# Performance work log

Hardware: AMD Instinct MI355X
Metric: run time of the kernel (lower is better)

## Reference

```python
import jax, jax.numpy as jnp
import numpy as np

B, S = 8192, 4096
EPS = 1e-6
ALPHA, BETA = 0.1, 0.1


def setup_inputs() -> dict:
    key = jax.random.key(0)
    k1, k2, k3, k4 = jax.random.split(key, 4)
    yhat = jax.random.normal(k1, (B, S), dtype=jnp.float32)
    y_dense = jax.random.normal(k2, (B, S), dtype=jnp.float32)
    keep = jax.random.bernoulli(k3, 0.5, (B, S))
    y = jnp.where(keep, y_dense, 0.0)
    # neighbor matrix: entries remapped {1.0->alpha, 2.0->beta}, mostly zero
    r = jax.random.randint(k4, (S, S), 0, 10)
    W = jnp.where(r == 1, ALPHA, jnp.where(r == 2, BETA, 0.0)).astype(jnp.float32)
    return {"yhat": yhat, "y": y, "W": W}


def reference(yhat, y, W):
    mask = (y != 0).astype(yhat.dtype)            # [B, S] nonzero-target mask
    sq = jnp.square(y - yhat)                      # [B, S] squared error
    # per-column loop `df_spatial_loss[:, i] = squared_error @ W[i]` == sq @ W.T
    spatial = sq @ W.T                             # [B, S] spatial regularization
    total = (sq + spatial) * mask                  # gather-at-nonzero == masking
    # mean over the nonzero entries only, then sqrt (RMSE)
    loss = jnp.sqrt(total.sum() / mask.sum() + EPS)
    return loss
```

## Files before the change

kernel.cpp:

```cpp
#include <hip/hip_runtime.h>
#include <math.h>

typedef unsigned long long u64;
typedef unsigned int u32;
typedef unsigned char u8;
typedef __attribute__((ext_vector_type(2))) unsigned long long u64x2;
typedef __attribute__((ext_vector_type(4))) int i32x4;

#define NB 8192
#define NS 4096

static const size_t OFF_CNT = 0;
static const size_t OFF_P3  = 16384;
static const size_t OFF_MB  = 32768;
static const size_t OFF_WB  = OFF_MB + (size_t)64 * 8192 * 8;
static const size_t OFF_M8  = 32768;
static const size_t OFF_BT  = OFF_M8 + (size_t)NB * NS;
static const size_t WS_NEED = OFF_BT + (size_t)NS * NS;

__device__ __forceinline__ void gload_lds16(const void* g, void* l) {
    __builtin_amdgcn_global_load_lds(
        (const __attribute__((address_space(1))) unsigned int*)g,
        (__attribute__((address_space(3))) unsigned int*)l, 16, 0, 0);
}


__global__ __launch_bounds__(256) void k1b_mask8(
    const float* __restrict__ y, u32* __restrict__ m8, u64* __restrict__ pcnt)
{
    __shared__ unsigned rc[4];
    const int t = threadIdx.x;
    const float4* y4 = (const float4*)y;
    size_t base = (size_t)blockIdx.x * 4096 + t;
    unsigned lcnt = 0;
    #pragma unroll 4
    for (int k = 0; k < 16; ++k) {
        float4 v = y4[base + (size_t)k * 256];
        unsigned b0 = v.x != 0.0f, b1 = v.y != 0.0f, b2 = v.z != 0.0f, b3 = v.w != 0.0f;
        lcnt += b0 + b1 + b2 + b3;
        m8[base + (size_t)k * 256] = b0 | (b1 << 8) | (b2 << 16) | (b3 << 24);
    }
    for (int off = 32; off; off >>= 1) lcnt += __shfl_down(lcnt, off, 64);
    if ((t & 63) == 0) rc[t >> 6] = lcnt;
    __syncthreads();
    if (t == 0) pcnt[blockIdx.x] = (u64)rc[0] + rc[1] + rc[2] + rc[3];
}

__global__ __launch_bounds__(256) void k2b_bt(
    const float* __restrict__ W, u32* __restrict__ bt)
{
    __shared__ float tile[64][65];
    const int j0 = blockIdx.x * 64, i0 = blockIdx.y * 64;
    const int t = threadIdx.x;
    #pragma unroll
    for (int k = 0; k < 16; ++k) {
        int lin = t + (k << 8);
        int r = lin >> 6, c = lin & 63;
        tile[r][c] = W[(size_t)(i0 + r) * NS + (j0 + c)];
    }
    __syncthreads();
    const int jj = t >> 2, ck = t & 3;
    u32 wd[4];
    #pragma unroll
    for (int g = 0; g < 4; ++g) {
        u32 u = 0;
        #pragma unroll
        for (int bb = 0; bb < 4; ++bb)
            u |= (tile[ck * 16 + g * 4 + bb][jj] != 0.0f ? 1u : 0u) << (8 * bb);
        wd[g] = u;
    }
    uint4 out = make_uint4(wd[0], wd[1], wd[2], wd[3]);
    *(uint4*)&bt[(((size_t)(j0 + jj) << 12) + (size_t)(i0 + ck * 16)) >> 2] = out;
}

__global__ __launch_bounds__(256) void k3b_mfma(
    const float* __restrict__ y, const float* __restrict__ yhat,
    const u8* __restrict__ m8, const u8* __restrict__ bt,
    double* __restrict__ p3)
{
    __shared__ alignas(16) u8 lds[2][16384];
    const int b0 = blockIdx.x << 7;
    const int j0 = blockIdx.y << 7;
    const int t = threadIdx.x, l = t & 63, wv = t >> 6;
    const int wr = wv >> 1, wc = wv & 1;

    const int row4 = t >> 2, pos = t & 3;
    const int chunk = pos ^ ((row4 >> 1) & 3);
    const u8* srcA = m8 + ((size_t)(b0 + row4) << 12) + ((size_t)chunk << 4);
    const u8* srcB = bt + ((size_t)(j0 + row4) << 12) + ((size_t)chunk << 4);

    const int slot = ((l >> 4) ^ ((l >> 1) & 3)) & 3;
    const int frbase = ((wr << 6) + (l & 15)) * 64 + (slot << 4);
    const int fcbase = 8192 + ((wc << 6) + (l & 15)) * 64 + (slot << 4);

    i32x4 acc[4][4];
    #pragma unroll
    for (int i = 0; i < 4; ++i)
        #pragma unroll
        for (int j = 0; j < 4; ++j) acc[i][j] = (i32x4){0, 0, 0, 0};

    auto stage = [&](int s, int buf) {
        const u8* sA = srcA + (s << 6);
        const u8* sB = srcB + (s << 6);
        u8* dA = &lds[buf][(size_t)wv << 10];
        u8* dB = &lds[buf][8192 + ((size_t)wv << 10)];
        gload_lds16(sA, dA);
        gload_lds16(sA + ((size_t)64 << 12), dA + 4096);
        gload_lds16(sB, dB);
        gload_lds16(sB + ((size_t)64 << 12), dB + 4096);
    };

    stage(0, 0);
    __syncthreads();

    #pragma unroll 1
    for (int ks = 0; ks < 64; ++ks) {
        const int cb = ks & 1;
        if (ks < 63) stage(ks + 1, cb ^ 1);
        const u8* L = lds[cb];
        i32x4 a[4], b[4];
        #pragma unroll
        for (int f = 0; f < 4; ++f) {
            a[f] = *(const i32x4*)&L[frbase + f * 1024];
            b[f] = *(const i32x4*)&L[fcbase + f * 1024];
        }
        #pragma unroll
        for (int fr = 0; fr < 4; ++fr)
            #pragma unroll
            for (int fc = 0; fc < 4; ++fc)
                acc[fr][fc] = __builtin_amdgcn_mfma_i32_16x16x64_i8(
                    a[fr], b[fc], acc[fr][fc], 0, 0, 0);
        __syncthreads();
    }

    float part = 0.0f;
    const int col = j0 + (wc << 6) + (l & 15);
    #pragma unroll
    for (int fr = 0; fr < 4; ++fr)
        #pragma unroll
        for (int q = 0; q < 4; ++q) {
            size_t rbase = ((size_t)(b0 + (wr << 6) + (fr << 4) + ((l >> 4) << 2) + q) << 12) + col;
            #pragma unroll
            for (int fc = 0; fc < 4; ++fc) {
                float yv = y[rbase + (fc << 4)];
                float hv = yhat[rbase + (fc << 4)];
                float e = yv - hv;
                float wgt = 0.1f * (float)acc[fr][fc][q] + (yv != 0.0f ? 1.0f : 0.0f);
                part = fmaf(e * e, wgt, part);
            }
        }

    for (int off = 32; off; off >>= 1) part += __shfl_down(part, off, 64);
    float* red = (float*)lds;
    __syncthreads();
    if ((t & 63) == 0) red[t >> 6] = part;
    __syncthreads();
    if (t == 0)
        p3[(size_t)blockIdx.y * gridDim.x + blockIdx.x] =
            (double)red[0] + (double)red[1] + (double)red[2] + (double)red[3];
}


__global__ __launch_bounds__(256) void k1_pack_mask(
    const float* __restrict__ y, u64* __restrict__ mbT, u64* __restrict__ pcnt)
{
    __shared__ unsigned rc[4];
    const unsigned t = threadIdx.x;
    const unsigned lane = t & 63;
    const float4* y4 = (const float4*)y;
    u64 qi = (u64)blockIdx.x * 256 + t;
    const u64 stride = (u64)2048 * 256;
    unsigned lcnt = 0;
    #pragma unroll 4
    for (int it = 0; it < 16; ++it, qi += stride) {
        float4 v = y4[qi];
        u64 b0 = __ballot(v.x != 0.0f);
        u64 b1 = __ballot(v.y != 0.0f);
        u64 b2 = __ballot(v.z != 0.0f);
        u64 b3 = __ballot(v.w != 0.0f);
        lcnt += (v.x != 0.0f) + (v.y != 0.0f) + (v.z != 0.0f) + (v.w != 0.0f);
        if (lane < 4) {
            unsigned sh = lane << 4;
            u64 word = ((b0 >> sh) & 0xFFFFull)
                     | (((b1 >> sh) & 0xFFFFull) << 16)
                     | (((b2 >> sh) & 0xFFFFull) << 32)
                     | (((b3 >> sh) & 0xFFFFull) << 48);
            u64 gw = ((qi - lane) >> 4) + lane;
            mbT[((gw & 63) << 13) + (gw >> 6)] = word;
        }
    }
    for (int off = 32; off; off >>= 1) lcnt += __shfl_down(lcnt, off, 64);
    if ((t & 63) == 0) rc[t >> 6] = lcnt;
    __syncthreads();
    if (t == 0) pcnt[blockIdx.x] = (u64)rc[0] + rc[1] + rc[2] + rc[3];
}

__global__ __launch_bounds__(256) void k2_pack_w(
    const float* __restrict__ W, u64* __restrict__ wbT)
{
    __shared__ float tile[64][65];
    const int j0 = blockIdx.x * 64;
    const int w  = blockIdx.y;
    const int i0 = w * 64;
    const int t = threadIdx.x;
    #pragma unroll
    for (int k = 0; k < 16; ++k) {
        int lin = t + (k << 8);
        int r = lin >> 6, c = lin & 63;
        tile[r][c] = W[(size_t)(i0 + r) * NS + (j0 + c)];
    }
    __syncthreads();
    const int lane = t & 63;
    const int wvv = t >> 6;
    const int pr = ((lane & 15) << 2) + (lane >> 4);
    for (int jj = wvv; jj < 64; jj += 4) {
        u64 bal = __ballot(tile[pr][jj] != 0.0f);
        if (lane == 0) wbT[((size_t)w << 12) + (j0 + jj)] = bal;
    }
}

__global__ __launch_bounds__(256) void k3_main(
    const float* __restrict__ y, const float* __restrict__ yhat,
    const u64* __restrict__ mbT, const u64* __restrict__ wbT,
    double* __restrict__ p3)
{
    __shared__ alignas(16) u64 mT[16 * 128];
    __shared__ alignas(16) u64 wT[16 * 128];
    const int b0 = blockIdx.x << 7;
    const int j0 = blockIdx.y << 7;
    const int t  = threadIdx.x;
    const int r0 = (t >> 4) << 3;
    const int cj = t & 15;
    const unsigned sx = ((unsigned)cj >> 2) << 4;

    unsigned cnt[8][8];
    #pragma unroll
    for (int a = 0; a < 8; ++a)
        #pragma unroll
        for (int b = 0; b < 8; ++b) cnt[a][b] = 0;

    char* mB = (char*)mT;
    char* wB = (char*)wT;

    #pragma unroll 1
    for (int s = 0; s < 4; ++s) {
        u64x2 gm[4], gq[4];
        #pragma unroll
        for (int k = 0; k < 4; ++k) {
            int lin = t + (k << 8);
            int wl = (s << 4) + (lin >> 6), c2 = lin & 63;
            gm[k] = *(const u64x2*)&mbT[((size_t)wl << 13) + b0 + 2 * c2];
            gq[k] = *(const u64x2*)&wbT[((size_t)wl << 12) + j0 + 2 * c2];
        }
        __syncthreads();
        #pragma unroll
        for (int k = 0; k < 4; ++k) {
            int lin = t + (k << 8);
            int wl = lin >> 6, c2 = lin & 63;
            int p = c2 ^ ((c2 >> 4) & 3);
            *(u64x2*)(mB + (wl << 10) + (c2 << 4)) = gm[k];
            *(u64x2*)(wB + (wl << 10) + (p << 4)) = gq[k];
        }
        __syncthreads();

        unsigned mo = (unsigned)(r0 << 3);
        unsigned qs = (unsigned)(cj << 6) + sx;
        #pragma unroll 2
        for (int w = 0; w < 16; ++w) {
            unsigned ml[16], ql[16];
            #pragma unroll
            for (int k = 0; k < 4; ++k) {
                uint4 a = *(const uint4*)(mB + mo + (k << 4));
                ml[4 * k + 0] = a.x; ml[4 * k + 1] = a.y;
                ml[4 * k + 2] = a.z; ml[4 * k + 3] = a.w;
                uint4 b = *(const uint4*)(wB + (qs ^ (unsigned)(k << 4)));
                ql[4 * k + 0] = b.x; ql[4 * k + 1] = b.y;
                ql[4 * k + 2] = b.z; ql[4 * k + 3] = b.w;
            }
            #pragma unroll
            for (int aa = 0; aa < 8; ++aa)
                #pragma unroll
                for (int bb = 0; bb < 8; ++bb) {
                    unsigned x0 = ml[2 * aa] & ql[2 * bb];
                    unsigned x1 = ml[2 * aa + 1] & ql[2 * bb + 1];
                    asm("v_bcnt_u32_b32 %0, %1, %0" : "+v"(cnt[aa][bb]) : "v"(x0));
                    asm("v_bcnt_u32_b32 %0, %1, %0" : "+v"(cnt[aa][bb]) : "v"(x1));
                }
            mo += 1024; qs += 1024;
        }
    }

    float part = 0.0f;
    const int c0 = cj << 3;
    #pragma unroll
    for (int aa = 0; aa < 8; ++aa) {
        size_t off = ((size_t)(b0 + r0 + aa) << 12) + (size_t)(j0 + c0);
        float ys[8], hs[8];
        *(float4*)&ys[0] = *(const float4*)(y + off);
        *(float4*)&ys[4] = *(const float4*)(y + off + 4);
        *(float4*)&hs[0] = *(const float4*)(yhat + off);
        *(float4*)&hs[4] = *(const float4*)(yhat + off + 4);
        #pragma unroll
        for (int bb = 0; bb < 8; ++bb) {
            float e = ys[bb] - hs[bb];
            float wgt = 0.1f * (float)cnt[aa][bb] + (ys[bb] != 0.0f ? 1.0f : 0.0f);
            part = fmaf(e * e, wgt, part);
        }
    }

    for (int off = 32; off; off >>= 1) part += __shfl_down(part, off, 64);
    float* red = (float*)mT;
    __syncthreads();
    if ((t & 63) == 0) red[t >> 6] = part;
    __syncthreads();
    if (t == 0)
        p3[(size_t)blockIdx.y * gridDim.x + blockIdx.x] =
            (double)red[0] + (double)red[1] + (double)red[2] + (double)red[3];
}

__global__ __launch_bounds__(256) void k4_final(
    const u64* __restrict__ pcnt, const double* __restrict__ p3, float* __restrict__ out)
{
    __shared__ double rs[4];
    __shared__ u64 rcc[4];
    double s3 = 0.0;
    u64 c = 0;
    for (int i = threadIdx.x; i < 2048; i += 256) { s3 += p3[i]; c += pcnt[i]; }
    for (int off = 32; off; off >>= 1) {
        s3 += __shfl_down(s3, off, 64);
        c  += __shfl_down(c, off, 64);
    }
    int wv = threadIdx.x >> 6;
    if ((threadIdx.x & 63) == 0) { rs[wv] = s3; rcc[wv] = c; }
    __syncthreads();
    if (threadIdx.x == 0) {
        double S3 = rs[0] + rs[1] + rs[2] + rs[3];
        double C  = (double)(rcc[0] + rcc[1] + rcc[2] + rcc[3]);
        out[0] = (float)sqrt(S3 / C + 1e-6);
    }
}

extern "C" void kernel_launch(void* const* d_in, const int* in_sizes, int n_in,
                              void* d_out, int out_size, void* d_ws, size_t ws_size,
                              hipStream_t stream) {
    const float* yhat = (const float*)d_in[0];
    const float* y    = (const float*)d_in[1];
    const float* W    = (const float*)d_in[2];
    char* ws = (char*)d_ws;
    u64*    pcnt = (u64*)(ws + OFF_CNT);
    double* p3   = (double*)(ws + OFF_P3);

    if (ws_size >= WS_NEED) {
        u32* m8 = (u32*)(ws + OFF_M8);
        u32* bt = (u32*)(ws + OFF_BT);
        k1b_mask8<<<dim3(2048), dim3(256), 0, stream>>>(y, m8, pcnt);
        k2b_bt<<<dim3(64, 64), dim3(256), 0, stream>>>(W, bt);
        k3b_mfma<<<dim3(64, 32), dim3(256), 0, stream>>>(
            y, yhat, (const u8*)m8, (const u8*)bt, p3);
        k4_final<<<dim3(1), dim3(256), 0, stream>>>(pcnt, p3, (float*)d_out);
    } else {
        u64* mbT = (u64*)(ws + OFF_MB);
        u64* wbT = (u64*)(ws + OFF_WB);
        k1_pack_mask<<<dim3(2048), dim3(256), 0, stream>>>(y, mbT, pcnt);
        k2_pack_w<<<dim3(64, 64), dim3(256), 0, stream>>>(W, wbT);
        k3_main<<<dim3(64, 32), dim3(256), 0, stream>>>(y, yhat, mbT, wbT, p3);
        k4_final<<<dim3(1), dim3(256), 0, stream>>>(pcnt, p3, (float*)d_out);
    }
}
```

Before: 226.2 us.

## Split output tiles between int8 MFMA and bit-popcount paths in one hybrid kernel

```diff
diff --git a/kernel.cpp b/kernel.cpp
--- a/kernel.cpp
+++ b/kernel.cpp
@@ -12,16 +12,284 @@
 
 static const size_t OFF_CNT = 0;
 static const size_t OFF_P3  = 16384;
-static const size_t OFF_MB  = 32768;
-static const size_t OFF_WB  = OFF_MB + (size_t)64 * 8192 * 8;
 static const size_t OFF_M8  = 32768;
 static const size_t OFF_BT  = OFF_M8 + (size_t)NB * NS;
-static const size_t WS_NEED = OFF_BT + (size_t)NS * NS;
+static const size_t WS_MFMA = OFF_BT + (size_t)NS * NS;
+static const size_t OFF_MBT = WS_MFMA;
+static const size_t OFF_WBT = OFF_MBT + (size_t)64 * NB * 8;
+static const size_t WS_HYB  = OFF_WBT + (size_t)64 * NS * 8;
 
 __device__ __forceinline__ void gload_lds16(const void* g, void* l) {
     __builtin_amdgcn_global_load_lds(
         (const __attribute__((address_space(1))) unsigned int*)g,
         (__attribute__((address_space(3))) unsigned int*)l, 16, 0, 0);
+}
+
+
+__global__ __launch_bounds__(256) void k1h(
+    const float* __restrict__ y, u32* __restrict__ m8,
+    u64* __restrict__ mbT, u64* __restrict__ pcnt)
+{
+    __shared__ unsigned rc[4];
+    const unsigned t = threadIdx.x;
+    const unsigned lane = t & 63;
+    const float4* y4 = (const float4*)y;
+    u64 qi = (u64)blockIdx.x * 256 + t;
+    const u64 stride = (u64)2048 * 256;
+    unsigned lcnt = 0;
+    #pragma unroll 4
+    for (int it = 0; it < 16; ++it, qi += stride) {
+        float4 v = y4[qi];
+        unsigned c0 = v.x != 0.0f, c1 = v.y != 0.0f, c2 = v.z != 0.0f, c3 = v.w != 0.0f;
+        u64 b0 = __ballot(v.x != 0.0f);
+        u64 b1 = __ballot(v.y != 0.0f);
+        u64 b2 = __ballot(v.z != 0.0f);
+        u64 b3 = __ballot(v.w != 0.0f);
+        lcnt += c0 + c1 + c2 + c3;
+        m8[qi] = c0 | (c1 << 8) | (c2 << 16) | (c3 << 24);
+        if (lane < 4) {
+            unsigned sh = lane << 4;
+            u64 word = ((b0 >> sh) & 0xFFFFull)
+                     | (((b1 >> sh) & 0xFFFFull) << 16)
+                     | (((b2 >> sh) & 0xFFFFull) << 32)
+                     | (((b3 >> sh) & 0xFFFFull) << 48);
+            u64 gw = ((qi - lane) >> 4) + lane;
+            mbT[((gw & 63) << 13) + (gw >> 6)] = word;
+        }
+    }
+    for (int off = 32; off; off >>= 1) lcnt += __shfl_down(lcnt, off, 64);
+    if ((t & 63) == 0) rc[t >> 6] = lcnt;
+    __syncthreads();
+    if (t == 0) pcnt[blockIdx.x] = (u64)rc[0] + rc[1] + rc[2] + rc[3];
+}
+
+__global__ __launch_bounds__(256) void k2h(
+    const float* __restrict__ W, u32* __restrict__ bt, u64* __restrict__ wbT)
+{
+    __shared__ float tile[64][65];
+    const int j0 = blockIdx.x * 64, w = blockIdx.y, i0 = w * 64;
+    const int t = threadIdx.x;
+    #pragma unroll
+    for (int k = 0; k < 16; ++k) {
+        int lin = t + (k << 8);
+        int r = lin >> 6, c = lin & 63;
+        tile[r][c] = W[(size_t)(i0 + r) * NS + (j0 + c)];
+    }
+    __syncthreads();
+    {
+        const int jj = t >> 2, ck = t & 3;
+        u32 wd[4];
+        #pragma unroll
+        for (int g = 0; g < 4; ++g) {
+            u32 u = 0;
+            #pragma unroll
+            for (int bb = 0; bb < 4; ++bb)
+                u |= (tile[ck * 16 + g * 4 + bb][jj] != 0.0f ? 1u : 0u) << (8 * bb);
+            wd[g] = u;
+        }
+        uint4 out = make_uint4(wd[0], wd[1], wd[2], wd[3]);
+        *(uint4*)&bt[(((size_t)(j0 + jj) << 12) + (size_t)(i0 + ck * 16)) >> 2] = out;
+    }
+    {
+        const int lane = t & 63;
+        const int wvv = t >> 6;
+        const int pr = ((lane & 15) << 2) + (lane >> 4);
+        for (int jj = wvv; jj < 64; jj += 4) {
+            u64 bal = __ballot(tile[pr][jj] != 0.0f);
+            if (lane == 0) wbT[((size_t)w << 12) + (j0 + jj)] = bal;
+        }
+    }
+}
+
+__global__ __launch_bounds__(256) void k3h(
+    const float* __restrict__ y, const float* __restrict__ yhat,
+    const u8* __restrict__ m8, const u8* __restrict__ bt,
+    const u64* __restrict__ mbT, const u64* __restrict__ wbT,
+    double* __restrict__ p3)
+{
+    __shared__ alignas(16) u8 smem[32768];
+    const int g = blockIdx.x;
+    const int msel = g & 31;
+    const int t = threadIdx.x;
+
+    if (msel < 19) {
+        const int id = (g >> 5) * 19 + msel;
+        const int bx = id & 63, jy = id >> 6;
+        const int b0 = bx << 7;
+        const int j0 = jy << 7;
+        const int l = t & 63, wv = t >> 6;
+        const int wr = wv >> 1, wc = wv & 1;
+
+        const int row4 = t >> 2, pos = t & 3;
+        const int chunk = pos ^ ((row4 >> 1) & 3);
+        const u8* srcA = m8 + ((size_t)(b0 + row4) << 12) + ((size_t)chunk << 4);
+        const u8* srcB = bt + ((size_t)(j0 + row4) << 12) + ((size_t)chunk << 4);
+
+        const int slot = ((l >> 4) ^ ((l >> 1) & 3)) & 3;
+        const int frbase = ((wr << 6) + (l & 15)) * 64 + (slot << 4);
+        const int fcbase = 8192 + ((wc << 6) + (l & 15)) * 64 + (slot << 4);
+
+        i32x4 acc[4][4];
+        #pragma unroll
+        for (int i = 0; i < 4; ++i)
+            #pragma unroll
+            for (int j = 0; j < 4; ++j) acc[i][j] = (i32x4){0, 0, 0, 0};
+
+        u8* const buf0 = smem;
+        u8* const buf1 = smem + 16384;
+
+        auto stage = [&](int s, u8* base) {
+            const u8* sA = srcA + (s << 6);
+            const u8* sB = srcB + (s << 6);
+            u8* dA = base + ((size_t)wv << 10);
+            u8* dB = base + 8192 + ((size_t)wv << 10);
+            gload_lds16(sA, dA);
+            gload_lds16(sA + ((size_t)64 << 12), dA + 4096);
+            gload_lds16(sB, dB);
+            gload_lds16(sB + ((size_t)64 << 12), dB + 4096);
+        };
+
+        stage(0, buf0);
+        __syncthreads();
+
+        #pragma unroll 1
+        for (int ks = 0; ks < 64; ++ks) {
+            u8* cb = (ks & 1) ? buf1 : buf0;
+            u8* nb = (ks & 1) ? buf0 : buf1;
+            if (ks < 63) stage(ks + 1, nb);
+            i32x4 a[4], b[4];
+            #pragma unroll
+            for (int f = 0; f < 4; ++f) {
+                a[f] = *(const i32x4*)&cb[frbase + f * 1024];
+                b[f] = *(const i32x4*)&cb[fcbase + f * 1024];
+            }
+            #pragma unroll
+            for (int fr = 0; fr < 4; ++fr)
+                #pragma unroll
+                for (int fc = 0; fc < 4; ++fc)
+                    acc[fr][fc] = __builtin_amdgcn_mfma_i32_16x16x64_i8(
+                        a[fr], b[fc], acc[fr][fc], 0, 0, 0);
+            __syncthreads();
+        }
+
+        float part = 0.0f;
+        const int col = j0 + (wc << 6) + (l & 15);
+        #pragma unroll
+        for (int fr = 0; fr < 4; ++fr)
+            #pragma unroll
+            for (int q = 0; q < 4; ++q) {
+                size_t rbase = ((size_t)(b0 + (wr << 6) + (fr << 4) + ((l >> 4) << 2) + q) << 12) + col;
+                #pragma unroll
+                for (int fc = 0; fc < 4; ++fc) {
+                    float yv = y[rbase + (fc << 4)];
+                    float hv = yhat[rbase + (fc << 4)];
+                    float e = yv - hv;
+                    float wgt = 0.1f * (float)acc[fr][fc][q] + (yv != 0.0f ? 1.0f : 0.0f);
+                    part = fmaf(e * e, wgt, part);
+                }
+            }
+
+        for (int off = 32; off; off >>= 1) part += __shfl_down(part, off, 64);
+        float* red = (float*)smem;
+        __syncthreads();
+        if ((t & 63) == 0) red[t >> 6] = part;
+        __syncthreads();
+        if (t == 0)
+            p3[(size_t)jy * 64 + bx] =
+                (double)red[0] + (double)red[1] + (double)red[2] + (double)red[3];
+    } else {
+        const int id = (g >> 5) * 13 + (msel - 19);
+        const int bx = id & 63, jy = 19 + (id >> 6);
+        const int b0 = bx << 7;
+        const int j0 = jy << 7;
+        const int r0 = (t >> 4) << 3;
+        const int cj = t & 15;
+        const unsigned sx = ((unsigned)cj >> 2) << 4;
+
+        unsigned cnt[8][8];
+        #pragma unroll
+        for (int a = 0; a < 8; ++a)
+            #pragma unroll
+            for (int b = 0; b < 8; ++b) cnt[a][b] = 0;
+
+        char* mB = (char*)smem;
+        char* wB = (char*)(smem + 16384);
+
+        #pragma unroll 1
+        for (int s = 0; s < 4; ++s) {
+            u64x2 gm[4], gq[4];
+            #pragma unroll
+            for (int k = 0; k < 4; ++k) {
+                int lin = t + (k << 8);
+                int wl = (s << 4) + (lin >> 6), c2 = lin & 63;
+                gm[k] = *(const u64x2*)&mbT[((size_t)wl << 13) + b0 + 2 * c2];
+                gq[k] = *(const u64x2*)&wbT[((size_t)wl << 12) + j0 + 2 * c2];
+            }
+            __syncthreads();
+            #pragma unroll
+            for (int k = 0; k < 4; ++k) {
+                int lin = t + (k << 8);
+                int wl = lin >> 6, c2 = lin & 63;
+                int p = c2 ^ ((c2 >> 4) & 3);
+                *(u64x2*)(mB + (wl << 10) + (c2 << 4)) = gm[k];
+                *(u64x2*)(wB + (wl << 10) + (p << 4)) = gq[k];
+            }
+            __syncthreads();
+
+            unsigned mo = (unsigned)(r0 << 3);
+            unsigned qs = (unsigned)(cj << 6) + sx;
+            #pragma unroll 2
+            for (int w = 0; w < 16; ++w) {
+                unsigned ml[16], ql[16];
+                #pragma unroll
+                for (int k = 0; k < 4; ++k) {
+                    uint4 a = *(const uint4*)(mB + mo + (k << 4));
+                    ml[4 * k + 0] = a.x; ml[4 * k + 1] = a.y;
+                    ml[4 * k + 2] = a.z; ml[4 * k + 3] = a.w;
+                    uint4 b = *(const uint4*)(wB + (qs ^ (unsigned)(k << 4)));
+                    ql[4 * k + 0] = b.x; ql[4 * k + 1] = b.y;
+                    ql[4 * k + 2] = b.z; ql[4 * k + 3] = b.w;
+                }
+                #pragma unroll
+                for (int aa = 0; aa < 8; ++aa)
+                    #pragma unroll
+                    for (int bb = 0; bb < 8; ++bb) {
+                        unsigned x0 = ml[2 * aa] & ql[2 * bb];
+                        unsigned x1 = ml[2 * aa + 1] & ql[2 * bb + 1];
+                        asm("v_bcnt_u32_b32 %0, %1, %0" : "+v"(cnt[aa][bb]) : "v"(x0));
+                        asm("v_bcnt_u32_b32 %0, %1, %0" : "+v"(cnt[aa][bb]) : "v"(x1));
+                    }
+                mo += 1024; qs += 1024;
+            }
+        }
+
+        float part = 0.0f;
+        const int c0 = cj << 3;
+        #pragma unroll
+        for (int aa = 0; aa < 8; ++aa) {
+            size_t off = ((size_t)(b0 + r0 + aa) << 12) + (size_t)(j0 + c0);
+            float ys[8], hs[8];
+            *(float4*)&ys[0] = *(const float4*)(y + off);
+            *(float4*)&ys[4] = *(const float4*)(y + off + 4);
+            *(float4*)&hs[0] = *(const float4*)(yhat + off);
+            *(float4*)&hs[4] = *(const float4*)(yhat + off + 4);
+            #pragma unroll
+            for (int bb = 0; bb < 8; ++bb) {
+                float e = ys[bb] - hs[bb];
+                float wgt = 0.1f * (float)cnt[aa][bb] + (ys[bb] != 0.0f ? 1.0f : 0.0f);
+                part = fmaf(e * e, wgt, part);
+            }
+        }
+
+        for (int off = 32; off; off >>= 1) part += __shfl_down(part, off, 64);
+        float* red = (float*)smem;
+        __syncthreads();
+        if ((t & 63) == 0) red[t >> 6] = part;
+        __syncthreads();
+        if (t == 0)
+            p3[(size_t)jy * 64 + bx] =
+                (double)red[0] + (double)red[1] + (double)red[2] + (double)red[3];
+    }
 }
 
 
@@ -160,164 +428,6 @@
             (double)red[0] + (double)red[1] + (double)red[2] + (double)red[3];
 }
 
-
-__global__ __launch_bounds__(256) void k1_pack_mask(
-    const float* __restrict__ y, u64* __restrict__ mbT, u64* __restrict__ pcnt)
-{
-    __shared__ unsigned rc[4];
-    const unsigned t = threadIdx.x;
-    const unsigned lane = t & 63;
-    const float4* y4 = (const float4*)y;
-    u64 qi = (u64)blockIdx.x * 256 + t;
-    const u64 stride = (u64)2048 * 256;
-    unsigned lcnt = 0;
-    #pragma unroll 4
-    for (int it = 0; it < 16; ++it, qi += stride) {
-        float4 v = y4[qi];
-        u64 b0 = __ballot(v.x != 0.0f);
-        u64 b1 = __ballot(v.y != 0.0f);
-        u64 b2 = __ballot(v.z != 0.0f);
-        u64 b3 = __ballot(v.w != 0.0f);
-        lcnt += (v.x != 0.0f) + (v.y != 0.0f) + (v.z != 0.0f) + (v.w != 0.0f);
-        if (lane < 4) {
-            unsigned sh = lane << 4;
-            u64 word = ((b0 >> sh) & 0xFFFFull)
-                     | (((b1 >> sh) & 0xFFFFull) << 16)
-                     | (((b2 >> sh) & 0xFFFFull) << 32)
-                     | (((b3 >> sh) & 0xFFFFull) << 48);
-            u64 gw = ((qi - lane) >> 4) + lane;
-            mbT[((gw & 63) << 13) + (gw >> 6)] = word;
-        }
-    }
-    for (int off = 32; off; off >>= 1) lcnt += __shfl_down(lcnt, off, 64);
-    if ((t & 63) == 0) rc[t >> 6] = lcnt;
-    __syncthreads();
-    if (t == 0) pcnt[blockIdx.x] = (u64)rc[0] + rc[1] + rc[2] + rc[3];
-}
-
-__global__ __launch_bounds__(256) void k2_pack_w(
-    const float* __restrict__ W, u64* __restrict__ wbT)
-{
-    __shared__ float tile[64][65];
-    const int j0 = blockIdx.x * 64;
-    const int w  = blockIdx.y;
-    const int i0 = w * 64;
-    const int t = threadIdx.x;
-    #pragma unroll
-    for (int k = 0; k < 16; ++k) {
-        int lin = t + (k << 8);
-        int r = lin >> 6, c = lin & 63;
-        tile[r][c] = W[(size_t)(i0 + r) * NS + (j0 + c)];
-    }
-    __syncthreads();
-    const int lane = t & 63;
-    const int wvv = t >> 6;
-    const int pr = ((lane & 15) << 2) + (lane >> 4);
-    for (int jj = wvv; jj < 64; jj += 4) {
-        u64 bal = __ballot(tile[pr][jj] != 0.0f);
-        if (lane == 0) wbT[((size_t)w << 12) + (j0 + jj)] = bal;
-    }
-}
-
-__global__ __launch_bounds__(256) void k3_main(
-    const float* __restrict__ y, const float* __restrict__ yhat,
-    const u64* __restrict__ mbT, const u64* __restrict__ wbT,
-    double* __restrict__ p3)
-{
-    __shared__ alignas(16) u64 mT[16 * 128];
-    __shared__ alignas(16) u64 wT[16 * 128];
-    const int b0 = blockIdx.x << 7;
-    const int j0 = blockIdx.y << 7;
-    const int t  = threadIdx.x;
-    const int r0 = (t >> 4) << 3;
-    const int cj = t & 15;
-    const unsigned sx = ((unsigned)cj >> 2) << 4;
-
-    unsigned cnt[8][8];
-    #pragma unroll
-    for (int a = 0; a < 8; ++a)
-        #pragma unroll
-        for (int b = 0; b < 8; ++b) cnt[a][b] = 0;
-
-    char* mB = (char*)mT;
-    char* wB = (char*)wT;
-
-    #pragma unroll 1
-    for (int s = 0; s < 4; ++s) {
-        u64x2 gm[4], gq[4];
-        #pragma unroll
-        for (int k = 0; k < 4; ++k) {
-            int lin = t + (k << 8);
-            int wl = (s << 4) + (lin >> 6), c2 = lin & 63;
-            gm[k] = *(const u64x2*)&mbT[((size_t)wl << 13) + b0 + 2 * c2];
-            gq[k] = *(const u64x2*)&wbT[((size_t)wl << 12) + j0 + 2 * c2];
-        }
-        __syncthreads();
-        #pragma unroll
-        for (int k = 0; k < 4; ++k) {
-            int lin = t + (k << 8);
-            int wl = lin >> 6, c2 = lin & 63;
-            int p = c2 ^ ((c2 >> 4) & 3);
-            *(u64x2*)(mB + (wl << 10) + (c2 << 4)) = gm[k];
-            *(u64x2*)(wB + (wl << 10) + (p << 4)) = gq[k];
-        }
-        __syncthreads();
-
-        unsigned mo = (unsigned)(r0 << 3);
-        unsigned qs = (unsigned)(cj << 6) + sx;
-        #pragma unroll 2
-        for (int w = 0; w < 16; ++w) {
-            unsigned ml[16], ql[16];
-            #pragma unroll
-            for (int k = 0; k < 4; ++k) {
-                uint4 a = *(const uint4*)(mB + mo + (k << 4));
-                ml[4 * k + 0] = a.x; ml[4 * k + 1] = a.y;
-                ml[4 * k + 2] = a.z; ml[4 * k + 3] = a.w;
-                uint4 b = *(const uint4*)(wB + (qs ^ (unsigned)(k << 4)));
-                ql[4 * k + 0] = b.x; ql[4 * k + 1] = b.y;
-                ql[4 * k + 2] = b.z; ql[4 * k + 3] = b.w;
-            }
-            #pragma unroll
-            for (int aa = 0; aa < 8; ++aa)
-                #pragma unroll
-                for (int bb = 0; bb < 8; ++bb) {
-                    unsigned x0 = ml[2 * aa] & ql[2 * bb];
-                    unsigned x1 = ml[2 * aa + 1] & ql[2 * bb + 1];
-                    asm("v_bcnt_u32_b32 %0, %1, %0" : "+v"(cnt[aa][bb]) : "v"(x0));
-                    asm("v_bcnt_u32_b32 %0, %1, %0" : "+v"(cnt[aa][bb]) : "v"(x1));
-                }
-            mo += 1024; qs += 1024;
-        }
-    }
-
-    float part = 0.0f;
-    const int c0 = cj << 3;
-    #pragma unroll
-    for (int aa = 0; aa < 8; ++aa) {
-        size_t off = ((size_t)(b0 + r0 + aa) << 12) + (size_t)(j0 + c0);
-        float ys[8], hs[8];
-        *(float4*)&ys[0] = *(const float4*)(y + off);
-        *(float4*)&ys[4] = *(const float4*)(y + off + 4);
-        *(float4*)&hs[0] = *(const float4*)(yhat + off);
-        *(float4*)&hs[4] = *(const float4*)(yhat + off + 4);
-        #pragma unroll
-        for (int bb = 0; bb < 8; ++bb) {
-            float e = ys[bb] - hs[bb];
-            float wgt = 0.1f * (float)cnt[aa][bb] + (ys[bb] != 0.0f ? 1.0f : 0.0f);
-            part = fmaf(e * e, wgt, part);
-        }
-    }
-
-    for (int off = 32; off; off >>= 1) part += __shfl_down(part, off, 64);
-    float* red = (float*)mT;
-    __syncthreads();
-    if ((t & 63) == 0) red[t >> 6] = part;
-    __syncthreads();
-    if (t == 0)
-        p3[(size_t)blockIdx.y * gridDim.x + blockIdx.x] =
-            (double)red[0] + (double)red[1] + (double)red[2] + (double)red[3];
-}
-
 __global__ __launch_bounds__(256) void k4_final(
     const u64* __restrict__ pcnt, const double* __restrict__ p3, float* __restrict__ out)
 {
@@ -349,21 +459,22 @@
     char* ws = (char*)d_ws;
     u64*    pcnt = (u64*)(ws + OFF_CNT);
     double* p3   = (double*)(ws + OFF_P3);
-
-    if (ws_size >= WS_NEED) {
-        u32* m8 = (u32*)(ws + OFF_M8);
-        u32* bt = (u32*)(ws + OFF_BT);
+    u32*    m8   = (u32*)(ws + OFF_M8);
+    u32*    bt   = (u32*)(ws + OFF_BT);
+
+    if (ws_size >= WS_HYB) {
+        u64* mbT = (u64*)(ws + OFF_MBT);
+        u64* wbT = (u64*)(ws + OFF_WBT);
+        k1h<<<dim3(2048), dim3(256), 0, stream>>>(y, m8, mbT, pcnt);
+        k2h<<<dim3(64, 64), dim3(256), 0, stream>>>(W, bt, wbT);
+        k3h<<<dim3(2048), dim3(256), 0, stream>>>(
+            y, yhat, (const u8*)m8, (const u8*)bt, mbT, wbT, p3);
+        k4_final<<<dim3(1), dim3(256), 0, stream>>>(pcnt, p3, (float*)d_out);
+    } else {
         k1b_mask8<<<dim3(2048), dim3(256), 0, stream>>>(y, m8, pcnt);
         k2b_bt<<<dim3(64, 64), dim3(256), 0, stream>>>(W, bt);
         k3b_mfma<<<dim3(64, 32), dim3(256), 0, stream>>>(
             y, yhat, (const u8*)m8, (const u8*)bt, p3);
         k4_final<<<dim3(1), dim3(256), 0, stream>>>(pcnt, p3, (float*)d_out);
-    } else {
-        u64* mbT = (u64*)(ws + OFF_MB);
-        u64* wbT = (u64*)(ws + OFF_WB);
-        k1_pack_mask<<<dim3(2048), dim3(256), 0, stream>>>(y, mbT, pcnt);
-        k2_pack_w<<<dim3(64, 64), dim3(256), 0, stream>>>(W, wbT);
-        k3_main<<<dim3(64, 32), dim3(256), 0, stream>>>(y, yhat, mbT, wbT, p3);
-        k4_final<<<dim3(1), dim3(256), 0, stream>>>(pcnt, p3, (float*)d_out);
-    }
-}
+    }
+}
```

After: 306.7 us. 1.36x slower.

## Merge prep kernels and load A fragments directly from global into registers

Applied to the files above, without the earlier changes.

```diff
diff --git a/kernel.cpp b/kernel.cpp
--- a/kernel.cpp
+++ b/kernel.cpp
@@ -12,11 +12,11 @@
 
 static const size_t OFF_CNT = 0;
 static const size_t OFF_P3  = 16384;
-static const size_t OFF_MB  = 32768;
-static const size_t OFF_WB  = OFF_MB + (size_t)64 * 8192 * 8;
 static const size_t OFF_M8  = 32768;
 static const size_t OFF_BT  = OFF_M8 + (size_t)NB * NS;
 static const size_t WS_NEED = OFF_BT + (size_t)NS * NS;
+static const size_t OFF_MB  = 32768;
+static const size_t OFF_WB  = OFF_MB + (size_t)64 * NB * 8;
 
 __device__ __forceinline__ void gload_lds16(const void* g, void* l) {
     __builtin_amdgcn_global_load_lds(
@@ -25,60 +25,60 @@
 }
 
 
-__global__ __launch_bounds__(256) void k1b_mask8(
-    const float* __restrict__ y, u32* __restrict__ m8, u64* __restrict__ pcnt)
-{
-    __shared__ unsigned rc[4];
+__global__ __launch_bounds__(256) void k12_prep(
+    const float* __restrict__ y, const float* __restrict__ W,
+    u32* __restrict__ m8, u32* __restrict__ bt, u64* __restrict__ pcnt)
+{
+    const int g = blockIdx.x;
     const int t = threadIdx.x;
-    const float4* y4 = (const float4*)y;
-    size_t base = (size_t)blockIdx.x * 4096 + t;
-    unsigned lcnt = 0;
-    #pragma unroll 4
-    for (int k = 0; k < 16; ++k) {
-        float4 v = y4[base + (size_t)k * 256];
-        unsigned b0 = v.x != 0.0f, b1 = v.y != 0.0f, b2 = v.z != 0.0f, b3 = v.w != 0.0f;
-        lcnt += b0 + b1 + b2 + b3;
-        m8[base + (size_t)k * 256] = b0 | (b1 << 8) | (b2 << 16) | (b3 << 24);
-    }
-    for (int off = 32; off; off >>= 1) lcnt += __shfl_down(lcnt, off, 64);
-    if ((t & 63) == 0) rc[t >> 6] = lcnt;
-    __syncthreads();
-    if (t == 0) pcnt[blockIdx.x] = (u64)rc[0] + rc[1] + rc[2] + rc[3];
-}
-
-__global__ __launch_bounds__(256) void k2b_bt(
-    const float* __restrict__ W, u32* __restrict__ bt)
-{
-    __shared__ float tile[64][65];
-    const int j0 = blockIdx.x * 64, i0 = blockIdx.y * 64;
-    const int t = threadIdx.x;
-    #pragma unroll
-    for (int k = 0; k < 16; ++k) {
-        int lin = t + (k << 8);
-        int r = lin >> 6, c = lin & 63;
-        tile[r][c] = W[(size_t)(i0 + r) * NS + (j0 + c)];
-    }
-    __syncthreads();
-    const int jj = t >> 2, ck = t & 3;
-    u32 wd[4];
-    #pragma unroll
-    for (int g = 0; g < 4; ++g) {
-        u32 u = 0;
-        #pragma unroll
-        for (int bb = 0; bb < 4; ++bb)
-            u |= (tile[ck * 16 + g * 4 + bb][jj] != 0.0f ? 1u : 0u) << (8 * bb);
-        wd[g] = u;
-    }
-    uint4 out = make_uint4(wd[0], wd[1], wd[2], wd[3]);
-    *(uint4*)&bt[(((size_t)(j0 + jj) << 12) + (size_t)(i0 + ck * 16)) >> 2] = out;
-}
-
-__global__ __launch_bounds__(256) void k3b_mfma(
+    if (g < 2048) {
+        __shared__ unsigned rc[4];
+        const float4* y4 = (const float4*)y;
+        size_t base = (size_t)g * 4096 + t;
+        unsigned lcnt = 0;
+        #pragma unroll 4
+        for (int k = 0; k < 16; ++k) {
+            float4 v = y4[base + (size_t)k * 256];
+            unsigned b0 = v.x != 0.0f, b1 = v.y != 0.0f, b2 = v.z != 0.0f, b3 = v.w != 0.0f;
+            lcnt += b0 + b1 + b2 + b3;
+            m8[base + (size_t)k * 256] = b0 | (b1 << 8) | (b2 << 16) | (b3 << 24);
+        }
+        for (int off = 32; off; off >>= 1) lcnt += __shfl_down(lcnt, off, 64);
+        if ((t & 63) == 0) rc[t >> 6] = lcnt;
+        __syncthreads();
+        if (t == 0) pcnt[g] = (u64)rc[0] + rc[1] + rc[2] + rc[3];
+    } else {
+        __shared__ float tile[64][65];
+        const int gg = g - 2048;
+        const int j0 = (gg & 63) * 64, i0 = (gg >> 6) * 64;
+        #pragma unroll
+        for (int k = 0; k < 16; ++k) {
+            int lin = t + (k << 8);
+            int r = lin >> 6, c = lin & 63;
+            tile[r][c] = W[(size_t)(i0 + r) * NS + (j0 + c)];
+        }
+        __syncthreads();
+        const int jj = t >> 2, ck = t & 3;
+        u32 wd[4];
+        #pragma unroll
+        for (int gq = 0; gq < 4; ++gq) {
+            u32 u = 0;
+            #pragma unroll
+            for (int bb = 0; bb < 4; ++bb)
+                u |= (tile[ck * 16 + gq * 4 + bb][jj] != 0.0f ? 1u : 0u) << (8 * bb);
+            wd[gq] = u;
+        }
+        uint4 out = make_uint4(wd[0], wd[1], wd[2], wd[3]);
+        *(uint4*)&bt[(((size_t)(j0 + jj) << 12) + (size_t)(i0 + ck * 16)) >> 2] = out;
+    }
+}
+
+__global__ __launch_bounds__(256) void k3f_mfma(
     const float* __restrict__ y, const float* __restrict__ yhat,
     const u8* __restrict__ m8, const u8* __restrict__ bt,
     double* __restrict__ p3)
 {
-    __shared__ alignas(16) u8 lds[2][16384];
+    __shared__ alignas(16) u8 lds[2][8192];
     const int b0 = blockIdx.x << 7;
     const int j0 = blockIdx.y << 7;
     const int t = threadIdx.x, l = t & 63, wv = t >> 6;
@@ -86,12 +86,12 @@
 
     const int row4 = t >> 2, pos = t & 3;
     const int chunk = pos ^ ((row4 >> 1) & 3);
-    const u8* srcA = m8 + ((size_t)(b0 + row4) << 12) + ((size_t)chunk << 4);
     const u8* srcB = bt + ((size_t)(j0 + row4) << 12) + ((size_t)chunk << 4);
 
     const int slot = ((l >> 4) ^ ((l >> 1) & 3)) & 3;
-    const int frbase = ((wr << 6) + (l & 15)) * 64 + (slot << 4);
-    const int fcbase = 8192 + ((wc << 6) + (l & 15)) * 64 + (slot << 4);
+    const int fcbase = ((wc << 6) + (l & 15)) * 64 + (slot << 4);
+
+    const u8* srcA = m8 + ((size_t)(b0 + (wr << 6) + (l & 15)) << 12) + ((l >> 4) << 4);
 
     i32x4 acc[4][4];
     #pragma unroll
@@ -99,37 +99,41 @@
         #pragma unroll
         for (int j = 0; j < 4; ++j) acc[i][j] = (i32x4){0, 0, 0, 0};
 
-    auto stage = [&](int s, int buf) {
-        const u8* sA = srcA + (s << 6);
+    auto stageB = [&](int s, int buf) {
         const u8* sB = srcB + (s << 6);
-        u8* dA = &lds[buf][(size_t)wv << 10];
-        u8* dB = &lds[buf][8192 + ((size_t)wv << 10)];
-        gload_lds16(sA, dA);
-        gload_lds16(sA + ((size_t)64 << 12), dA + 4096);
+        u8* dB = &lds[buf][(size_t)wv << 10];
         gload_lds16(sB, dB);
         gload_lds16(sB + ((size_t)64 << 12), dB + 4096);
     };
 
-    stage(0, 0);
+    i32x4 aN[4];
+    auto loadA = [&](int s, i32x4* dst) {
+        #pragma unroll
+        for (int fr = 0; fr < 4; ++fr)
+            dst[fr] = *(const i32x4*)(srcA + ((size_t)fr << 16) + (s << 6));
+    };
+
+    stageB(0, 0);
+    loadA(0, aN);
     __syncthreads();
 
     #pragma unroll 1
     for (int ks = 0; ks < 64; ++ks) {
         const int cb = ks & 1;
-        if (ks < 63) stage(ks + 1, cb ^ 1);
+        i32x4 aC[4];
+        #pragma unroll
+        for (int f = 0; f < 4; ++f) aC[f] = aN[f];
+        if (ks < 63) { stageB(ks + 1, cb ^ 1); loadA(ks + 1, aN); }
         const u8* L = lds[cb];
-        i32x4 a[4], b[4];
-        #pragma unroll
-        for (int f = 0; f < 4; ++f) {
-            a[f] = *(const i32x4*)&L[frbase + f * 1024];
-            b[f] = *(const i32x4*)&L[fcbase + f * 1024];
-        }
+        i32x4 b[4];
+        #pragma unroll
+        for (int f = 0; f < 4; ++f) b[f] = *(const i32x4*)&L[fcbase + f * 1024];
         #pragma unroll
         for (int fr = 0; fr < 4; ++fr)
             #pragma unroll
             for (int fc = 0; fc < 4; ++fc)
                 acc[fr][fc] = __builtin_amdgcn_mfma_i32_16x16x64_i8(
-                    a[fr], b[fc], acc[fr][fc], 0, 0, 0);
+                    aC[fr], b[fc], acc[fr][fc], 0, 0, 0);
         __syncthreads();
     }
 
@@ -353,9 +357,8 @@
     if (ws_size >= WS_NEED) {
         u32* m8 = (u32*)(ws + OFF_M8);
         u32* bt = (u32*)(ws + OFF_BT);
-        k1b_mask8<<<dim3(2048), dim3(256), 0, stream>>>(y, m8, pcnt);
-        k2b_bt<<<dim3(64, 64), dim3(256), 0, stream>>>(W, bt);
-        k3b_mfma<<<dim3(64, 32), dim3(256), 0, stream>>>(
+        k12_prep<<<dim3(2048 + 4096), dim3(256), 0, stream>>>(y, W, m8, bt, pcnt);
+        k3f_mfma<<<dim3(64, 32), dim3(256), 0, stream>>>(
             y, yhat, (const u8*)m8, (const u8*)bt, p3);
         k4_final<<<dim3(1), dim3(256), 0, stream>>>(pcnt, p3, (float*)d_out);
     } else {
```

New measurement: 345.2 us. 52.6% more time.
